# Kernel optimization log

Measured on AMD Instinct MI355X. Metric: run time of the kernel, lower is better.

## Reference

```python
import jax, jax.numpy as jnp
import numpy as np

NUM_SEGMENTS = 100000


def setup_inputs() -> dict:
    key = jax.random.key(0)
    k1, k2 = jax.random.split(key)
    x = jax.random.normal(k1, (4000000, 32), dtype=jnp.float32)
    index = jax.random.randint(k2, (4000000,), 0, NUM_SEGMENTS, dtype=jnp.int64)
    return {"x": x, "index": index}


def reference(x, index):
    # scatter_mean(x, index, dim=0): sum rows per segment, divide by count (clamped to 1)
    sums = jax.ops.segment_sum(x, index, num_segments=NUM_SEGMENTS)  # [S, D]
    counts = jax.ops.segment_sum(jnp.ones((x.shape[0],), dtype=x.dtype), index,
                                 num_segments=NUM_SEGMENTS)  # [S]
    return sums / jnp.maximum(counts, 1.0)[:, None]
```

## Files before the change

### kernel.cpp

```cpp
#include <hip/hip_runtime.h>

#define NSEG 100000
#define DIM 32

__global__ void scatter_sum_kernel(const float* __restrict__ x,
                                   const int* __restrict__ idx,
                                   float* __restrict__ sums,
                                   float* __restrict__ cnts,
                                   int n_elems) {
    int i = blockIdx.x * blockDim.x + threadIdx.x;
    if (i >= n_elems) return;
    int row = i >> 5;
    int col = i & 31;
    int seg = idx[row];
    atomicAdd(&sums[seg * DIM + col], x[i]);
    if (col == 0) {
        atomicAdd(&cnts[seg], 1.0f);
    }
}

__global__ void divide_kernel(float* __restrict__ out,
                              const float* __restrict__ cnts,
                              int n) {
    int i = blockIdx.x * blockDim.x + threadIdx.x;
    if (i >= n) return;
    float c = cnts[i >> 5];
    out[i] = out[i] / fmaxf(c, 1.0f);
}

extern "C" void kernel_launch(void* const* d_in, const int* in_sizes, int n_in,
                              void* d_out, int out_size, void* d_ws, size_t ws_size,
                              hipStream_t stream) {
    const float* x   = (const float*)d_in[0];
    const int*   idx = (const int*)d_in[1];
    float* out  = (float*)d_out;
    float* cnts = (float*)d_ws;

    int n_elems = in_sizes[0];

    hipMemsetAsync(d_out, 0, (size_t)out_size * sizeof(float), stream);
    hipMemsetAsync(d_ws, 0, (size_t)NSEG * sizeof(float), stream);

    const int threads = 256;
    int blocks = (n_elems + threads - 1) / threads;
    scatter_sum_kernel<<<blocks, threads, 0, stream>>>(x, idx, out, cnts, n_elems);

    int blocks2 = (out_size + threads - 1) / threads;
    divide_kernel<<<blocks2, threads, 0, stream>>>(out, cnts, out_size);
}
```

Before: 1.119 ms.

## Replace float atomic scatter with counting-sort gather segment reduction

Adds a counting sort of row ids by segment: histogram, three-kernel prefix scan, and an atomic cursor scatter of row indices. A per-segment wave kernel then gathers rows, reduces them in registers and writes the mean directly. This removes 128M float atomics and the separate divide pass, at the cost of several extra launches, int atomics over N, and scattered 128-byte row reads. The old path remains as a fallback when the workspace is too small, so whether the new path runs depends on the workspace size.

```diff
diff --git a/kernel.cpp b/kernel.cpp
--- a/kernel.cpp
+++ b/kernel.cpp
@@ -2,6 +2,91 @@
 
 #define NSEG 100000
 #define DIM 32
+#define SCAN_BLOCK 1024
+
+__global__ void hist_kernel(const int* __restrict__ idx, int* __restrict__ cnt, int n) {
+    int i = blockIdx.x * blockDim.x + threadIdx.x;
+    if (i < n) atomicAdd(&cnt[idx[i]], 1);
+}
+
+__global__ void scan_block_reduce(const int* __restrict__ cnt, int* __restrict__ bsums, int nseg) {
+    __shared__ int lds[SCAN_BLOCK];
+    int i = blockIdx.x * SCAN_BLOCK + threadIdx.x;
+    lds[threadIdx.x] = (i < nseg) ? cnt[i] : 0;
+    __syncthreads();
+    for (int off = SCAN_BLOCK / 2; off > 0; off >>= 1) {
+        if (threadIdx.x < off) lds[threadIdx.x] += lds[threadIdx.x + off];
+        __syncthreads();
+    }
+    if (threadIdx.x == 0) bsums[blockIdx.x] = lds[0];
+}
+
+__global__ void scan_bsums(int* __restrict__ bsums, int nb) {
+    __shared__ int lds[128];
+    int t = threadIdx.x;
+    int v = (t < nb) ? bsums[t] : 0;
+    lds[t] = v;
+    __syncthreads();
+    for (int off = 1; off < 128; off <<= 1) {
+        int add = (t >= off) ? lds[t - off] : 0;
+        __syncthreads();
+        lds[t] += add;
+        __syncthreads();
+    }
+    if (t < nb) bsums[t] = lds[t] - v;
+}
+
+__global__ void scan_final(const int* __restrict__ cnt, const int* __restrict__ bsums,
+                           int* __restrict__ offs, int* __restrict__ cursor, int nseg) {
+    __shared__ int lds[SCAN_BLOCK];
+    int t = threadIdx.x;
+    int i = blockIdx.x * SCAN_BLOCK + t;
+    int v = (i < nseg) ? cnt[i] : 0;
+    lds[t] = v;
+    __syncthreads();
+    for (int off = 1; off < SCAN_BLOCK; off <<= 1) {
+        int add = (t >= off) ? lds[t - off] : 0;
+        __syncthreads();
+        lds[t] += add;
+        __syncthreads();
+    }
+    if (i < nseg) {
+        int e = bsums[blockIdx.x] + lds[t] - v;
+        offs[i] = e;
+        cursor[i] = e;
+    }
+}
+
+__global__ void scatter_ids(const int* __restrict__ idx, int* __restrict__ cursor,
+                            int* __restrict__ rowid, int n) {
+    int i = blockIdx.x * blockDim.x + threadIdx.x;
+    if (i < n) {
+        int pos = atomicAdd(&cursor[idx[i]], 1);
+        rowid[pos] = i;
+    }
+}
+
+__global__ void seg_sum(const float* __restrict__ x, const int* __restrict__ rowid,
+                        const int* __restrict__ offs, const int* __restrict__ cnt,
+                        float* __restrict__ out, int nseg) {
+    int wave = threadIdx.x >> 6;
+    int lane = threadIdx.x & 63;
+    int seg = blockIdx.x * (blockDim.x >> 6) + wave;
+    if (seg >= nseg) return;
+    int start = offs[seg];
+    int count = cnt[seg];
+    int col = lane & 31;
+    int slot = lane >> 5;
+    float acc = 0.f;
+    for (int j = start + slot; j < start + count; j += 2) {
+        int r = rowid[j];
+        acc += x[(size_t)r * DIM + col];
+    }
+    acc += __shfl_down(acc, 32, 64);
+    if (slot == 0) {
+        out[(size_t)seg * DIM + col] = acc / fmaxf((float)count, 1.0f);
+    }
+}
 
 __global__ void scatter_sum_kernel(const float* __restrict__ x,
                                    const int* __restrict__ idx,
@@ -14,14 +99,10 @@
     int col = i & 31;
     int seg = idx[row];
     atomicAdd(&sums[seg * DIM + col], x[i]);
-    if (col == 0) {
-        atomicAdd(&cnts[seg], 1.0f);
-    }
+    if (col == 0) atomicAdd(&cnts[seg], 1.0f);
 }
 
-__global__ void divide_kernel(float* __restrict__ out,
-                              const float* __restrict__ cnts,
-                              int n) {
+__global__ void divide_kernel(float* __restrict__ out, const float* __restrict__ cnts, int n) {
     int i = blockIdx.x * blockDim.x + threadIdx.x;
     if (i >= n) return;
     float c = cnts[i >> 5];
@@ -33,18 +114,38 @@
                               hipStream_t stream) {
     const float* x   = (const float*)d_in[0];
     const int*   idx = (const int*)d_in[1];
-    float* out  = (float*)d_out;
-    float* cnts = (float*)d_ws;
+    float* out = (float*)d_out;
 
+    int N = in_sizes[1];
     int n_elems = in_sizes[0];
 
-    hipMemsetAsync(d_out, 0, (size_t)out_size * sizeof(float), stream);
-    hipMemsetAsync(d_ws, 0, (size_t)NSEG * sizeof(float), stream);
+    const int nb_scan = (NSEG + SCAN_BLOCK - 1) / SCAN_BLOCK;
+    size_t needed = (size_t)(3 * NSEG + 128 + N) * sizeof(int);
 
-    const int threads = 256;
-    int blocks = (n_elems + threads - 1) / threads;
-    scatter_sum_kernel<<<blocks, threads, 0, stream>>>(x, idx, out, cnts, n_elems);
+    if (ws_size < needed) {
+        float* cnts = (float*)d_ws;
+        hipMemsetAsync(d_out, 0, (size_t)out_size * sizeof(float), stream);
+        hipMemsetAsync(d_ws, 0, (size_t)NSEG * sizeof(float), stream);
+        int blocks = (n_elems + 255) / 256;
+        scatter_sum_kernel<<<blocks, 256, 0, stream>>>(x, idx, out, cnts, n_elems);
+        divide_kernel<<<(out_size + 255) / 256, 256, 0, stream>>>(out, cnts, out_size);
+        return;
+    }
 
-    int blocks2 = (out_size + threads - 1) / threads;
-    divide_kernel<<<blocks2, threads, 0, stream>>>(out, cnts, out_size);
+    int* cnt    = (int*)d_ws;
+    int* offs   = cnt + NSEG;
+    int* cursor = offs + NSEG;
+    int* bsums  = cursor + NSEG;
+    int* rowid  = bsums + 128;
+
+    hipMemsetAsync(cnt, 0, (size_t)NSEG * sizeof(int), stream);
+
+    hist_kernel<<<(N + 255) / 256, 256, 0, stream>>>(idx, cnt, N);
+    scan_block_reduce<<<nb_scan, SCAN_BLOCK, 0, stream>>>(cnt, bsums, NSEG);
+    scan_bsums<<<1, 128, 0, stream>>>(bsums, nb_scan);
+    scan_final<<<nb_scan, SCAN_BLOCK, 0, stream>>>(cnt, bsums, offs, cursor, NSEG);
+    scatter_ids<<<(N + 255) / 256, 256, 0, stream>>>(idx, cursor, rowid, N);
+
+    int segblocks = (NSEG + 3) / 4;
+    seg_sum<<<segblocks, 256, 0, stream>>>(x, rowid, offs, cnt, out, NSEG);
 }
```

After: 1.365 ms. 1.22x slower.
